# Performance work log

Measured on AMD Instinct MI355X. Metric: run time of the kernel, lower is better.

## Reference

```python
import jax, jax.numpy as jnp
import numpy as np

BN_EPS = 1e-5

# Octonion multiplication table: hamilton block (r, c) = SIGN[c][r] * a[IDX[c][r]]
IDX = np.array([
    [0,1,2,3,4,5,6,7],
    [1,0,3,2,5,4,7,6],
    [2,3,0,1,6,7,4,5],
    [3,2,1,0,7,6,5,4],
    [4,5,6,7,0,1,2,3],
    [5,4,7,6,1,0,3,2],
    [6,7,4,5,2,3,0,1],
    [7,6,5,4,3,2,1,0]], dtype=np.int32)
SIGN = np.array([
    [ 1, 1, 1, 1, 1, 1, 1, 1],
    [ 1,-1, 1,-1, 1,-1,-1, 1],
    [ 1,-1,-1, 1, 1, 1,-1,-1],
    [ 1, 1,-1,-1, 1,-1, 1,-1],
    [ 1,-1,-1,-1,-1, 1, 1, 1],
    [ 1, 1,-1, 1,-1,-1,-1, 1],
    [ 1, 1, 1,-1,-1, 1,-1,-1],
    [ 1,-1, 1, 1,-1,-1, 1,-1]], dtype=np.float32)

def make_octonion_mul(kernel):
    # kernel: [in/8, out]; split cols into 8 chunks a0..a7 of [in/8, out/8]
    in8, out = kernel.shape
    out8 = out // 8
    a = kernel.reshape(in8, 8, out8).transpose(1, 0, 2)  # [8, in/8, out/8]
    blocks = jnp.asarray(SIGN)[:, :, None, None] * a[jnp.asarray(IDX)]  # [c, r, in/8, out/8]
    # hamilton[r*in8:(r+1)*in8, c*out8:(c+1)*out8] = blocks[c, r]
    return jnp.transpose(blocks, (1, 2, 0, 3)).reshape(8 * in8, out)  # [in, out]

def setup_inputs() -> dict:
    key = jax.random.key(0)
    ks = jax.random.split(key, 5)
    N, E, D_IN, D_OUT = 100000, 3200000, 256, 256
    stdv = float(np.sqrt(6.0 / (D_IN // 8 + D_OUT)))
    return {
        "x": jax.random.normal(ks[0], (N, D_IN), dtype=jnp.float32),
        "weight": jax.random.uniform(ks[1], (D_IN // 8, D_OUT), dtype=jnp.float32,
                                      minval=-stdv, maxval=stdv),
        "gamma": jnp.ones((D_OUT,), dtype=jnp.float32),
        "beta": jnp.zeros((D_OUT,), dtype=jnp.float32),
        "edge_weight": jax.random.uniform(ks[2], (E,), dtype=jnp.float32),
        "edge_src": jax.random.randint(ks[3], (E,), 0, N, dtype=jnp.int32),
        "edge_dst": jax.random.randint(ks[4], (E,), 0, N, dtype=jnp.int32),
    }

def reference(x, weight, gamma, beta, edge_weight, edge_src, edge_dst):
    N = x.shape[0]
    hamilton = make_octonion_mul(weight)          # [in, out]
    support = x @ hamilton                        # [N, out]
    # sparse adjacency aggregation: out[dst] += w * support[src]
    msgs = edge_weight[:, None] * support[edge_src]
    out = jax.ops.segment_sum(msgs, edge_dst, num_segments=N)  # [N, out]
    # BatchNorm1d (training mode: batch stats, biased variance)
    mean = jnp.mean(out, axis=0)
    var = jnp.var(out, axis=0)
    out = (out - mean) * jax.lax.rsqrt(var + BN_EPS) * gamma + beta
    return jnp.tanh(out)
```

## Files before the change

kernel.cpp:

```cpp
#include <hip/hip_runtime.h>
#include <cmath>

#define NB 512
#define CHUNK 8192

typedef short short8 __attribute__((ext_vector_type(8)));
typedef float f32x4 __attribute__((ext_vector_type(4)));

__constant__ int c_IDX[64] = {
  0,1,2,3,4,5,6,7,
  1,0,3,2,5,4,7,6,
  2,3,0,1,6,7,4,5,
  3,2,1,0,7,6,5,4,
  4,5,6,7,0,1,2,3,
  5,4,7,6,1,0,3,2,
  6,7,4,5,2,3,0,1,
  7,6,5,4,3,2,1,0};
__constant__ float c_SIGN[64] = {
  1,1,1,1,1,1,1,1,
  1,-1,1,-1,1,-1,-1,1,
  1,-1,-1,1,1,1,-1,-1,
  1,1,-1,-1,1,-1,1,-1,
  1,-1,-1,-1,-1,1,1,1,
  1,1,-1,1,-1,-1,-1,1,
  1,1,1,-1,-1,1,-1,-1,
  1,-1,1,1,-1,-1,1,-1};

__device__ inline unsigned bf16_rne(float f) {
  unsigned u = __float_as_uint(f);
  return (u + 0x7fffu + ((u >> 16) & 1u)) >> 16;
}
__device__ inline unsigned bfpack(float lo, float hi) {
  return bf16_rne(lo) | (bf16_rne(hi) << 16);
}

__global__ __launch_bounds__(256) void hamT_kernel(const float* __restrict__ weight,
                                                   unsigned short* __restrict__ hi,
                                                   unsigned short* __restrict__ lo) {
  int idx = blockIdx.x * 256 + threadIdx.x;
  int col = idx >> 8, k = idx & 255;
  int r = k >> 5, i = k & 31, c = col >> 5, o = col & 31;
  float v = c_SIGN[c * 8 + r] * weight[i * 256 + c_IDX[c * 8 + r] * 32 + o];
  unsigned hb = bf16_rne(v);
  float hf = __uint_as_float(hb << 16);
  hi[idx] = (unsigned short)hb;
  lo[idx] = (unsigned short)bf16_rne(v - hf);
}

__global__ __launch_bounds__(256) void cvt_kernel(const float4* __restrict__ x4,
                                                  uint2* __restrict__ xh, size_t n4) {
  size_t idx = (size_t)blockIdx.x * 256 + threadIdx.x;
  size_t stride = (size_t)gridDim.x * 256;
  for (size_t i = idx; i < n4; i += stride) {
    float4 v = x4[i];
    xh[i] = make_uint2(bfpack(v.x, v.y), bfpack(v.z, v.w));
  }
}

__global__ __launch_bounds__(256) void binhist_kernel(const int* __restrict__ dst,
                                                      int* __restrict__ binTot,
                                                      int E, int N) {
  __shared__ int h[NB];
  int tid = threadIdx.x;
  for (int i = tid; i < NB; i += 256) h[i] = 0;
  __syncthreads();
  int base = blockIdx.x * CHUNK;
  int end = base + CHUNK; if (end > E) end = E;
  for (int i = base + tid; i < end; i += 256)
    atomicAdd(&h[(int)((long long)dst[i] * NB / N)], 1);
  __syncthreads();
  for (int i = tid; i < NB; i += 256)
    if (h[i]) atomicAdd(&binTot[i], h[i]);
}

__global__ __launch_bounds__(512) void binscan_kernel(const int* __restrict__ binTot,
                                                      int* __restrict__ binStart,
                                                      int* __restrict__ binCursor, int E) {
  __shared__ int wsum[8], wbase[8];
  int tid = threadIdx.x, lane = tid & 63, wid = tid >> 6;
  int v = binTot[tid];
  int incl = v;
  #pragma unroll
  for (int d = 1; d < 64; d <<= 1) { int u = __shfl_up(incl, d); if (lane >= d) incl += u; }
  if (lane == 63) wsum[wid] = incl;
  __syncthreads();
  if (tid == 0) { int s = 0; for (int w = 0; w < 8; w++) { wbase[w] = s; s += wsum[w]; } }
  __syncthreads();
  int excl = wbase[wid] + incl - v;
  binStart[tid] = excl;
  binCursor[tid] = excl;
  if (tid == NB - 1) binStart[NB] = E;
}

__global__ __launch_bounds__(256) void bin_scatter(const int* __restrict__ src,
                                                   const int* __restrict__ dst,
                                                   const float* __restrict__ w,
                                                   int* __restrict__ binCursor,
                                                   int2* __restrict__ bb, int E, int N) {
  __shared__ int hist[NB];
  __shared__ int lcur[NB];
  int tid = threadIdx.x;
  int base = blockIdx.x * CHUNK;
  int end = base + CHUNK; if (end > E) end = E;
  for (int i = tid; i < NB; i += 256) hist[i] = 0;
  __syncthreads();
  for (int i = base + tid; i < end; i += 256)
    atomicAdd(&hist[(int)((long long)dst[i] * NB / N)], 1);
  __syncthreads();
  for (int i = tid; i < NB; i += 256) {
    int h = hist[i];
    lcur[i] = h ? atomicAdd(&binCursor[i], h) : 0;
  }
  __syncthreads();
  for (int i = base + tid; i < end; i += 256) {
    int d = dst[i];
    int b = (int)((long long)d * NB / N);
    int d0 = (int)(((long long)b * N + NB - 1) / NB);
    int pos = atomicAdd(&lcur[b], 1);
    bb[pos] = make_int2(src[i] | ((d - d0) << 24), __float_as_int(w[i]));
  }
}

__global__ __launch_bounds__(256) void bin_place(const int2* __restrict__ bb,
                                                 const int* __restrict__ binStart,
                                                 int* __restrict__ off,
                                                 int* __restrict__ cnt,
                                                 int2* __restrict__ edges, int N) {
  __shared__ int lcnt[208];
  __shared__ int loff[208];
  int b = blockIdx.x, tid = threadIdx.x;
  int d0 = (int)(((long long)b * N + NB - 1) / NB);
  int d1 = (int)(((long long)(b + 1) * N + NB - 1) / NB);
  if (d1 > N) d1 = N;
  int nd = d1 - d0;
  int e0 = binStart[b], e1 = binStart[b + 1];
  for (int i = tid; i < nd; i += 256) lcnt[i] = 0;
  __syncthreads();
  for (int i = e0 + tid; i < e1; i += 256)
    atomicAdd(&lcnt[((unsigned)bb[i].x) >> 24], 1);
  __syncthreads();
  if (tid == 0) {
    int s = e0;
    for (int i = 0; i < nd; i++) { loff[i] = s; s += lcnt[i]; }
  }
  __syncthreads();
  for (int i = tid; i < nd; i += 256) {
    off[d0 + i] = loff[i];
    cnt[d0 + i] = lcnt[i];
  }
  __syncthreads();
  for (int i = tid; i < nd; i += 256) lcnt[i] = loff[i];
  __syncthreads();
  for (int i = e0 + tid; i < e1; i += 256) {
    int2 e = bb[i];
    int pos = atomicAdd(&lcnt[((unsigned)e.x) >> 24], 1);
    edges[pos] = make_int2(e.x & 0xFFFFFF, e.y);
  }
}

__device__ inline void acc8(float (&a)[8], uint4 v, float w) {
  a[0] = fmaf(w, __uint_as_float(v.x << 16), a[0]);
  a[1] = fmaf(w, __uint_as_float(v.x & 0xffff0000u), a[1]);
  a[2] = fmaf(w, __uint_as_float(v.y << 16), a[2]);
  a[3] = fmaf(w, __uint_as_float(v.y & 0xffff0000u), a[3]);
  a[4] = fmaf(w, __uint_as_float(v.z << 16), a[4]);
  a[5] = fmaf(w, __uint_as_float(v.z & 0xffff0000u), a[5]);
  a[6] = fmaf(w, __uint_as_float(v.w << 16), a[6]);
  a[7] = fmaf(w, __uint_as_float(v.w & 0xffff0000u), a[7]);
}

__global__ __launch_bounds__(256) void gather_kernel(const uint4* __restrict__ x16,
                                                     const int2* __restrict__ edges,
                                                     const int* __restrict__ off,
                                                     const int* __restrict__ cnt,
                                                     uint4* __restrict__ agg16, int N) {
  int d = blockIdx.x * 4 + (threadIdx.x >> 6);
  if (d >= N) return;
  int lane = threadIdx.x & 63;
  int h = lane >> 5, c = lane & 31;
  int start = off[d], n = cnt[d];
  float a[8] = {0.f, 0.f, 0.f, 0.f, 0.f, 0.f, 0.f, 0.f};
  int m = (n - h + 1) >> 1;
  int t = 0;
  for (; t + 1 < m; t += 2) {
    int2 e0 = edges[start + 2 * t + h];
    int2 e1 = edges[start + 2 * t + 2 + h];
    uint4 v0 = x16[(size_t)e0.x * 32 + c];
    uint4 v1 = x16[(size_t)e1.x * 32 + c];
    acc8(a, v0, __int_as_float(e0.y));
    acc8(a, v1, __int_as_float(e1.y));
  }
  if (t < m) {
    int2 e0 = edges[start + 2 * t + h];
    uint4 v0 = x16[(size_t)e0.x * 32 + c];
    acc8(a, v0, __int_as_float(e0.y));
  }
  #pragma unroll
  for (int i = 0; i < 8; i++) a[i] += __shfl_xor(a[i], 32);
  if (h == 0)
    agg16[(size_t)d * 32 + c] = make_uint4(bfpack(a[0], a[1]), bfpack(a[2], a[3]),
                                           bfpack(a[4], a[5]), bfpack(a[6], a[7]));
}

__global__ __launch_bounds__(512) void mfma_gemm(const uint4* __restrict__ aggh,
                                                 const unsigned short* __restrict__ hamT_hi,
                                                 const unsigned short* __restrict__ hamT_lo,
                                                 float* __restrict__ bnsum,
                                                 float* __restrict__ out, int N) {
  __shared__ __align__(16) unsigned short Al[128 * 256];
  __shared__ float csum[256], csq[256];
  const int tid = threadIdx.x;
  const int row0 = blockIdx.x * 128;
  const int lane = tid & 63, wv = tid >> 6;
  const int wm = wv >> 2, wn = wv & 3;

  if (tid < 256) { csum[tid] = 0.f; csq[tid] = 0.f; }

  #pragma unroll
  for (int it = 0; it < 8; it++) {
    int cidx = it * 512 + tid;
    int row = cidx >> 5, c16 = cidx & 31;
    int rg = row0 + row;
    uint4 v = make_uint4(0u, 0u, 0u, 0u);
    if (rg < N) v = aggh[(size_t)rg * 32 + c16];
    *(uint4*)((char*)Al + row * 512 + ((c16 * 16) ^ ((row & 7) << 4))) = v;
  }
  __syncthreads();

  f32x4 acc[4][4];
  #pragma unroll
  for (int m = 0; m < 4; m++)
    #pragma unroll
    for (int n = 0; n < 4; n++) acc[m][n] = (f32x4)0.f;

  const char* bh = (const char*)hamT_hi;
  const char* bl = (const char*)hamT_lo;
  #pragma unroll
  for (int kk = 0; kk < 8; kk++) {
    const int kbyte = (lane >> 4) * 16 + kk * 64;
    short8 af[4];
    #pragma unroll
    for (int m = 0; m < 4; m++) {
      int row = wm * 64 + m * 16 + (lane & 15);
      af[m] = *(const short8*)((const char*)Al + row * 512 + (kbyte ^ ((row & 7) << 4)));
    }
    #pragma unroll
    for (int n = 0; n < 4; n++) {
      int colg = wn * 64 + n * 16 + (lane & 15);
      size_t boff = (size_t)colg * 512 + kbyte;
      short8 bhv = *(const short8*)(bh + boff);
      short8 blv = *(const short8*)(bl + boff);
      #pragma unroll
      for (int m = 0; m < 4; m++)
        acc[m][n] = __builtin_amdgcn_mfma_f32_16x16x32_bf16(af[m], bhv, acc[m][n], 0, 0, 0);
      #pragma unroll
      for (int m = 0; m < 4; m++)
        acc[m][n] = __builtin_amdgcn_mfma_f32_16x16x32_bf16(af[m], blv, acc[m][n], 0, 0, 0);
    }
  }

  #pragma unroll
  for (int n = 0; n < 4; n++) {
    int colg = wn * 64 + n * 16 + (lane & 15);
    float s = 0.f, q = 0.f;
    #pragma unroll
    for (int m = 0; m < 4; m++) {
      int rgb = row0 + wm * 64 + m * 16 + (lane >> 4) * 4;
      #pragma unroll
      for (int r = 0; r < 4; r++) {
        float v = acc[m][n][r];
        s += v; q = fmaf(v, v, q);
        int rg = rgb + r;
        if (rg < N) out[(size_t)rg * 256 + colg] = v;
      }
    }
    s += __shfl_xor(s, 16); s += __shfl_xor(s, 32);
    q += __shfl_xor(q, 16); q += __shfl_xor(q, 32);
    if (lane < 16) {
      atomicAdd(&csum[wn * 64 + n * 16 + lane], s);
      atomicAdd(&csq [wn * 64 + n * 16 + lane], q);
    }
  }
  __syncthreads();
  if (tid < 256) {
    atomicAdd(&bnsum[tid], csum[tid]);
    atomicAdd(&bnsum[256 + tid], csq[tid]);
  }
}

__global__ void bnscale_kernel(const float* __restrict__ bnsum,
                               const float* __restrict__ gamma,
                               const float* __restrict__ beta,
                               float* __restrict__ bnsc, int N) {
  int c = threadIdx.x;
  float invN = 1.f / (float)N;
  float mean = bnsum[c] * invN;
  float var  = bnsum[256 + c] * invN - mean * mean;
  float sc = rsqrtf(var + 1e-5f) * gamma[c];
  bnsc[c] = sc;
  bnsc[256 + c] = beta[c] - mean * sc;
}

__global__ __launch_bounds__(256) void final_kernel(float* __restrict__ out,
                                                    const float* __restrict__ bnsc,
                                                    size_t total4) {
  size_t idx = (size_t)blockIdx.x * 256 + threadIdx.x;
  size_t stride = (size_t)gridDim.x * 256;
  float4* out4 = (float4*)out;
  for (size_t i = idx; i < total4; i += stride) {
    float4 v = out4[i];
    int c0 = (int)((i * 4) & 255);
    v.x = tanhf(fmaf(v.x, bnsc[c0 + 0], bnsc[256 + c0 + 0]));
    v.y = tanhf(fmaf(v.y, bnsc[c0 + 1], bnsc[256 + c0 + 1]));
    v.z = tanhf(fmaf(v.z, bnsc[c0 + 2], bnsc[256 + c0 + 2]));
    v.w = tanhf(fmaf(v.w, bnsc[c0 + 3], bnsc[256 + c0 + 3]));
    out4[i] = v;
  }
}

extern "C" void kernel_launch(void* const* d_in, const int* in_sizes, int n_in,
                              void* d_out, int out_size, void* d_ws, size_t ws_size,
                              hipStream_t stream) {
  const float* x      = (const float*)d_in[0];
  const float* weight = (const float*)d_in[1];
  const float* gamma  = (const float*)d_in[2];
  const float* beta   = (const float*)d_in[3];
  const float* ew     = (const float*)d_in[4];
  const int*   esrc   = (const int*)d_in[5];
  const int*   edst   = (const int*)d_in[6];
  const int N = in_sizes[0] / 256;
  const int E = in_sizes[4];
  float* out = (float*)d_out;

  char* p = (char*)d_ws;
  auto alloc = [&](size_t bytes) {
    char* q = p;
    p += (bytes + 255) & ~(size_t)255;
    return q;
  };
  unsigned short* hamT_hi = (unsigned short*)alloc(65536 * 2);
  unsigned short* hamT_lo = (unsigned short*)alloc(65536 * 2);
  int*   binTot    = (int*)alloc(NB * 4);
  int*   binStart  = (int*)alloc((NB + 1) * 4);
  int*   binCursor = (int*)alloc(NB * 4);
  int*   cnt       = (int*)alloc((size_t)N * 4);
  int*   off       = (int*)alloc((size_t)N * 4);
  int2*  bb        = (int2*)alloc((size_t)E * 8);
  int2*  edges     = (int2*)alloc((size_t)E * 8);
  uint2* xh        = (uint2*)alloc((size_t)N * 256 * 2);
  uint4* aggh      = (uint4*)alloc((size_t)N * 256 * 2);
  float* bnsum     = (float*)alloc(512 * 4);
  float* bnsc      = (float*)alloc(512 * 4);

  hipMemsetAsync(binTot, 0, NB * 4, stream);
  hipMemsetAsync(bnsum, 0, 512 * 4, stream);

  const int gridE = (E + CHUNK - 1) / CHUNK;
  const int rowBlocks = (N + 127) / 128;

  hamT_kernel<<<256, 256, 0, stream>>>(weight, hamT_hi, hamT_lo);
  cvt_kernel<<<2048, 256, 0, stream>>>((const float4*)x, xh, (size_t)N * 64);
  binhist_kernel<<<gridE, 256, 0, stream>>>(edst, binTot, E, N);
  binscan_kernel<<<1, 512, 0, stream>>>(binTot, binStart, binCursor, E);
  bin_scatter<<<gridE, 256, 0, stream>>>(esrc, edst, ew, binCursor, bb, E, N);
  bin_place<<<NB, 256, 0, stream>>>(bb, binStart, off, cnt, edges, N);
  gather_kernel<<<(N + 3) / 4, 256, 0, stream>>>((const uint4*)xh, edges, off, cnt, aggh, N);
  mfma_gemm<<<rowBlocks, 512, 0, stream>>>(aggh, hamT_hi, hamT_lo, bnsum, out, N);
  bnscale_kernel<<<1, 256, 0, stream>>>(bnsum, gamma, beta, bnsc, N);
  final_kernel<<<2048, 256, 0, stream>>>(out, bnsc, (size_t)N * 64);
}
```

Baseline: 521.0 us.

## Restructure gather to full-wave rows with 8-way edge unroll; fold BN scale into final

The gather kernel now gives each 64-lane wave a whole destination row, with each lane owning 4 bf16 columns (8-byte loads). It unrolls 8 edges per iteration instead of splitting edges across half-waves with 16-byte loads and a cross-half shuffle reduction. This aims to raise memory-level parallelism per wave and remove the shuffle. The BN scale/shift computation moves into the final kernel, precomputed per thread since the stride keeps the column fixed, which removes one tiny kernel launch. The risks are narrower per-lane loads and more register pressure from the unroll.

Measured after the change: 501.7 us. 3.7% less time.

```diff
diff --git a/kernel.cpp b/kernel.cpp
--- a/kernel.cpp
+++ b/kernel.cpp
@@ -158,48 +158,57 @@
   }
 }
 
-__device__ inline void acc8(float (&a)[8], uint4 v, float w) {
-  a[0] = fmaf(w, __uint_as_float(v.x << 16), a[0]);
-  a[1] = fmaf(w, __uint_as_float(v.x & 0xffff0000u), a[1]);
-  a[2] = fmaf(w, __uint_as_float(v.y << 16), a[2]);
-  a[3] = fmaf(w, __uint_as_float(v.y & 0xffff0000u), a[3]);
-  a[4] = fmaf(w, __uint_as_float(v.z << 16), a[4]);
-  a[5] = fmaf(w, __uint_as_float(v.z & 0xffff0000u), a[5]);
-  a[6] = fmaf(w, __uint_as_float(v.w << 16), a[6]);
-  a[7] = fmaf(w, __uint_as_float(v.w & 0xffff0000u), a[7]);
-}
-
-__global__ __launch_bounds__(256) void gather_kernel(const uint4* __restrict__ x16,
+__device__ inline void acc4(float& a0, float& a1, float& a2, float& a3,
+                            uint2 v, float w) {
+  a0 = fmaf(w, __uint_as_float(v.x << 16), a0);
+  a1 = fmaf(w, __uint_as_float(v.x & 0xffff0000u), a1);
+  a2 = fmaf(w, __uint_as_float(v.y << 16), a2);
+  a3 = fmaf(w, __uint_as_float(v.y & 0xffff0000u), a3);
+}
+
+__global__ __launch_bounds__(256) void gather_kernel(const uint2* __restrict__ x8,
                                                      const int2* __restrict__ edges,
                                                      const int* __restrict__ off,
                                                      const int* __restrict__ cnt,
-                                                     uint4* __restrict__ agg16, int N) {
+                                                     uint2* __restrict__ agg8, int N) {
   int d = blockIdx.x * 4 + (threadIdx.x >> 6);
   if (d >= N) return;
-  int lane = threadIdx.x & 63;
-  int h = lane >> 5, c = lane & 31;
+  int c = threadIdx.x & 63;
   int start = off[d], n = cnt[d];
-  float a[8] = {0.f, 0.f, 0.f, 0.f, 0.f, 0.f, 0.f, 0.f};
-  int m = (n - h + 1) >> 1;
+  float a0 = 0.f, a1 = 0.f, a2 = 0.f, a3 = 0.f;
   int t = 0;
-  for (; t + 1 < m; t += 2) {
-    int2 e0 = edges[start + 2 * t + h];
-    int2 e1 = edges[start + 2 * t + 2 + h];
-    uint4 v0 = x16[(size_t)e0.x * 32 + c];
-    uint4 v1 = x16[(size_t)e1.x * 32 + c];
-    acc8(a, v0, __int_as_float(e0.y));
-    acc8(a, v1, __int_as_float(e1.y));
-  }
-  if (t < m) {
-    int2 e0 = edges[start + 2 * t + h];
-    uint4 v0 = x16[(size_t)e0.x * 32 + c];
-    acc8(a, v0, __int_as_float(e0.y));
-  }
-  #pragma unroll
-  for (int i = 0; i < 8; i++) a[i] += __shfl_xor(a[i], 32);
-  if (h == 0)
-    agg16[(size_t)d * 32 + c] = make_uint4(bfpack(a[0], a[1]), bfpack(a[2], a[3]),
-                                           bfpack(a[4], a[5]), bfpack(a[6], a[7]));
+  for (; t + 8 <= n; t += 8) {
+    int2 e0 = edges[start + t + 0];
+    int2 e1 = edges[start + t + 1];
+    int2 e2 = edges[start + t + 2];
+    int2 e3 = edges[start + t + 3];
+    int2 e4 = edges[start + t + 4];
+    int2 e5 = edges[start + t + 5];
+    int2 e6 = edges[start + t + 6];
+    int2 e7 = edges[start + t + 7];
+    uint2 v0 = x8[(size_t)e0.x * 64 + c];
+    uint2 v1 = x8[(size_t)e1.x * 64 + c];
+    uint2 v2 = x8[(size_t)e2.x * 64 + c];
+    uint2 v3 = x8[(size_t)e3.x * 64 + c];
+    uint2 v4 = x8[(size_t)e4.x * 64 + c];
+    uint2 v5 = x8[(size_t)e5.x * 64 + c];
+    uint2 v6 = x8[(size_t)e6.x * 64 + c];
+    uint2 v7 = x8[(size_t)e7.x * 64 + c];
+    acc4(a0, a1, a2, a3, v0, __int_as_float(e0.y));
+    acc4(a0, a1, a2, a3, v1, __int_as_float(e1.y));
+    acc4(a0, a1, a2, a3, v2, __int_as_float(e2.y));
+    acc4(a0, a1, a2, a3, v3, __int_as_float(e3.y));
+    acc4(a0, a1, a2, a3, v4, __int_as_float(e4.y));
+    acc4(a0, a1, a2, a3, v5, __int_as_float(e5.y));
+    acc4(a0, a1, a2, a3, v6, __int_as_float(e6.y));
+    acc4(a0, a1, a2, a3, v7, __int_as_float(e7.y));
+  }
+  for (; t < n; t++) {
+    int2 e0 = edges[start + t];
+    uint2 v0 = x8[(size_t)e0.x * 64 + c];
+    acc4(a0, a1, a2, a3, v0, __int_as_float(e0.y));
+  }
+  agg8[(size_t)d * 64 + c] = make_uint2(bfpack(a0, a1), bfpack(a2, a3));
 }
 
 __global__ __launch_bounds__(512) void mfma_gemm(const uint4* __restrict__ aggh,
@@ -288,32 +297,30 @@
   }
 }
 
-__global__ void bnscale_kernel(const float* __restrict__ bnsum,
-                               const float* __restrict__ gamma,
-                               const float* __restrict__ beta,
-                               float* __restrict__ bnsc, int N) {
-  int c = threadIdx.x;
-  float invN = 1.f / (float)N;
-  float mean = bnsum[c] * invN;
-  float var  = bnsum[256 + c] * invN - mean * mean;
-  float sc = rsqrtf(var + 1e-5f) * gamma[c];
-  bnsc[c] = sc;
-  bnsc[256 + c] = beta[c] - mean * sc;
-}
-
 __global__ __launch_bounds__(256) void final_kernel(float* __restrict__ out,
-                                                    const float* __restrict__ bnsc,
-                                                    size_t total4) {
+                                                    const float* __restrict__ bnsum,
+                                                    const float* __restrict__ gamma,
+                                                    const float* __restrict__ beta,
+                                                    float invN, size_t total4) {
   size_t idx = (size_t)blockIdx.x * 256 + threadIdx.x;
   size_t stride = (size_t)gridDim.x * 256;
+  int c0 = (int)((idx * 4) & 255);
+  float sc[4], ofs[4];
+  #pragma unroll
+  for (int j = 0; j < 4; j++) {
+    float mean = bnsum[c0 + j] * invN;
+    float var  = bnsum[256 + c0 + j] * invN - mean * mean;
+    float s = rsqrtf(var + 1e-5f) * gamma[c0 + j];
+    sc[j] = s;
+    ofs[j] = beta[c0 + j] - mean * s;
+  }
   float4* out4 = (float4*)out;
   for (size_t i = idx; i < total4; i += stride) {
     float4 v = out4[i];
-    int c0 = (int)((i * 4) & 255);
-    v.x = tanhf(fmaf(v.x, bnsc[c0 + 0], bnsc[256 + c0 + 0]));
-    v.y = tanhf(fmaf(v.y, bnsc[c0 + 1], bnsc[256 + c0 + 1]));
-    v.z = tanhf(fmaf(v.z, bnsc[c0 + 2], bnsc[256 + c0 + 2]));
-    v.w = tanhf(fmaf(v.w, bnsc[c0 + 3], bnsc[256 + c0 + 3]));
+    v.x = tanhf(fmaf(v.x, sc[0], ofs[0]));
+    v.y = tanhf(fmaf(v.y, sc[1], ofs[1]));
+    v.z = tanhf(fmaf(v.z, sc[2], ofs[2]));
+    v.w = tanhf(fmaf(v.w, sc[3], ofs[3]));
     out4[i] = v;
   }
 }
@@ -350,7 +357,6 @@
   uint2* xh        = (uint2*)alloc((size_t)N * 256 * 2);
   uint4* aggh      = (uint4*)alloc((size_t)N * 256 * 2);
   float* bnsum     = (float*)alloc(512 * 4);
-  float* bnsc      = (float*)alloc(512 * 4);
 
   hipMemsetAsync(binTot, 0, NB * 4, stream);
   hipMemsetAsync(bnsum, 0, 512 * 4, stream);
@@ -364,8 +370,9 @@
   binscan_kernel<<<1, 512, 0, stream>>>(binTot, binStart, binCursor, E);
   bin_scatter<<<gridE, 256, 0, stream>>>(esrc, edst, ew, binCursor, bb, E, N);
   bin_place<<<NB, 256, 0, stream>>>(bb, binStart, off, cnt, edges, N);
-  gather_kernel<<<(N + 3) / 4, 256, 0, stream>>>((const uint4*)xh, edges, off, cnt, aggh, N);
+  gather_kernel<<<(N + 3) / 4, 256, 0, stream>>>((const uint2*)xh, edges, off, cnt,
+                                                 (uint2*)aggh, N);
   mfma_gemm<<<rowBlocks, 512, 0, stream>>>(aggh, hamT_hi, hamT_lo, bnsum, out, N);
-  bnscale_kernel<<<1, 256, 0, stream>>>(bnsum, gamma, beta, bnsc, N);
-  final_kernel<<<2048, 256, 0, stream>>>(out, bnsc, (size_t)N * 64);
-}
+  final_kernel<<<2048, 256, 0, stream>>>(out, bnsum, gamma, beta, 1.f / (float)N,
+                                         (size_t)N * 64);
+}
```
